# Kernel tuning notes

Hardware: AMD Instinct MI355X
Metric: run time of the kernel (lower is better)

Reference implementation:

```python
import jax, jax.numpy as jnp
import numpy as np
import math

S, D = 8192, 128

def setup_inputs() -> dict:
    key = jax.random.key(0)
    kq, kk, kv = jax.random.split(key, 3)
    return {
        "q": jax.random.normal(kq, (S, D), dtype=jnp.float32),
        "k": jax.random.normal(kk, (S, D), dtype=jnp.float32),
        "v": jax.random.normal(kv, (S, D), dtype=jnp.float32),
    }

def reference(q, k, v):
    # scores: [S, S]; scale by sqrt(d) as in the torch module
    scale = 1.0 / math.sqrt(q.shape[1])
    scores = (q @ k.T) * scale
    attn = jax.nn.softmax(scores, axis=-1)
    return attn @ v
```

## Files before the change

kernel.cpp:

```cpp
#include <hip/hip_runtime.h>
#include <hip/hip_bf16.h>

#define SEQ 8192
#define HD 128
#define BM 256
#define BN 64
#define NQT (SEQ / BM)
#define THREADS 1024

typedef __bf16 bf16_t;
typedef __bf16 bf16x2 __attribute__((ext_vector_type(2)));
typedef __bf16 bf16x8 __attribute__((ext_vector_type(8)));
typedef float f32x4 __attribute__((ext_vector_type(4)));
typedef float f32x16 __attribute__((ext_vector_type(16)));
typedef unsigned int u32x4 __attribute__((ext_vector_type(4)));

#if __has_builtin(__builtin_amdgcn_exp2f)
__device__ inline float exp2_fast(float x) { return __builtin_amdgcn_exp2f(x); }
#else
__device__ inline float exp2_fast(float x) { return exp2f(x); }
#endif

__device__ inline void load_lds16(const void* g, void* l) {
  __builtin_amdgcn_global_load_lds(
      (const __attribute__((address_space(1))) void*)g,
      (__attribute__((address_space(3))) void*)l, 16, 0, 0);
}

__global__ __launch_bounds__(256) void prep_kernel(const float* __restrict__ K,
                                                   const float* __restrict__ V,
                                                   bf16_t* __restrict__ Kb,
                                                   bf16_t* __restrict__ VT) {
  const int b = (int)blockIdx.x;
  const int tid = (int)threadIdx.x;
  if (b < 256) {
    __shared__ float tile[64][65];
    const int T = b & 127;
    const int d0 = (b >> 7) * 64;
    const int s0 = T * 64;
    const int r = tid >> 2;
    const int c0 = (tid & 3) * 16;
#pragma unroll
    for (int j4 = 0; j4 < 4; ++j4) {
      float4 x = *(const float4*)&V[(size_t)(s0 + r) * HD + d0 + c0 + j4 * 4];
      tile[r][c0 + j4 * 4 + 0] = x.x;
      tile[r][c0 + j4 * 4 + 1] = x.y;
      tile[r][c0 + j4 * 4 + 2] = x.z;
      tile[r][c0 + j4 * 4 + 3] = x.w;
    }
    __syncthreads();
    const int d_l = tid & 63;
    const int kc0 = (tid >> 6) * 2;
#pragma unroll
    for (int k2 = 0; k2 < 2; ++k2) {
      const int kc = kc0 + k2;
      bf16x8 wv;
#pragma unroll
      for (int j = 0; j < 8; ++j) wv[j] = (bf16_t)tile[kc * 8 + j][d_l];
      *(bf16x8*)&VT[((size_t)(T * 8 + kc) * 128 + d0 + d_l) * 8] = wv;
    }
  } else {
    const int base = (b - 256) * 2048 + tid * 8;
    const int row = base >> 7;
    const int c = (base >> 3) & 15;
    const int T = row >> 6;
    const int r = row & 63;
    float4 a = *(const float4*)&K[base];
    float4 cc = *(const float4*)&K[base + 4];
    bf16x8 f;
    f[0] = (bf16_t)a.x; f[1] = (bf16_t)a.y; f[2] = (bf16_t)a.z; f[3] = (bf16_t)a.w;
    f[4] = (bf16_t)cc.x; f[5] = (bf16_t)cc.y; f[6] = (bf16_t)cc.z; f[7] = (bf16_t)cc.w;
    *(bf16x8*)&Kb[((size_t)(T * 16 + c) * 64 + r) * 8] = f;
  }
}

__global__ __launch_bounds__(THREADS, 4) void fattn_kernel(
    const float* __restrict__ Q, const bf16_t* __restrict__ Kb,
    const bf16_t* __restrict__ VT, float* __restrict__ OpartT,
    float* __restrict__ Lpart, int kshift, int nit) {
  __shared__ __align__(16) bf16_t kt[2 * 8192];
  __shared__ __align__(16) bf16_t vt[3 * 8192];
  __shared__ __align__(16) char pbc[2 * 32768];

  const int tid = (int)threadIdx.x;
  const int lane = tid & 63;
  const int w = tid >> 6;
  const int qw = w & 7;
  const int g = w >> 3;
  const int h = lane >> 5;
  const int n32 = lane & 31;

  const int qt = (int)blockIdx.x >> kshift;
  const int sp = (int)blockIdx.x & ((1 << kshift) - 1);
  const int qbase = qt * BM;
  const int tile0 = sp * nit;

  const float SC2 = 0.08838834764831845f * 1.4426950408889634f;

  bf16x8 qf[8];
  {
    const float* qp = Q + (size_t)(qbase + qw * 32 + n32) * HD + h * 8;
#pragma unroll
    for (int kk = 0; kk < 8; ++kk) {
      float4 a = *(const float4*)(qp + kk * 16);
      float4 b = *(const float4*)(qp + kk * 16 + 4);
      bf16x8 f;
      f[0] = (bf16_t)(a.x * SC2); f[1] = (bf16_t)(a.y * SC2);
      f[2] = (bf16_t)(a.z * SC2); f[3] = (bf16_t)(a.w * SC2);
      f[4] = (bf16_t)(b.x * SC2); f[5] = (bf16_t)(b.y * SC2);
      f[6] = (bf16_t)(b.z * SC2); f[7] = (bf16_t)(b.w * SC2);
      qf[kk] = f;
    }
  }

  f32x16 o_acc[2];
#pragma unroll
  for (int i = 0; i < 2; ++i)
#pragma unroll
    for (int e = 0; e < 16; ++e) o_acc[i][e] = 0.f;
  float l_acc = 0.f;

  const bf16_t* ksrc = Kb + ((size_t)(tile0 * 16 + w) * 64 + lane) * 8;
  const bf16_t* vsrc = VT + ((size_t)(tile0 * 8 + (w >> 1)) * 128 + (w & 1) * 64 + lane) * 8;
  char* kdstb = (char*)kt + w * 1024;
  char* vdstb = (char*)vt + w * 1024;

  load_lds16(ksrc, kdstb);
  load_lds16(vsrc, vdstb);
  ksrc += 8192;
  vsrc += 8192;
  __syncthreads();

  const bf16_t* ktb = kt + (g * 32 + n32) * 8 + h * 512;
  const bf16_t* vtb = vt + (g * 64 + n32) * 8 + h * 1024;
  char* pbw = pbc + w * 2048 + lane * 16;
  const char* pbr = pbc + qw * 2048 + lane * 16;

  int kt_ro = 0;
  int ktd = 16384;
  int v_pv = 16384, v_nx = 0, v_fr = 8192;
  int p_wo = 0;

  for (int it = 0; it <= nit; ++it) {
    if (it + 1 < nit) {
      load_lds16(ksrc, kdstb + ktd);
      load_lds16(vsrc, vdstb + 2 * v_fr);
      ksrc += 8192;
      vsrc += 8192;
    }

    if (it < nit) {
      const bf16_t* kr = ktb + kt_ro;
      f32x16 sacc;
#pragma unroll
      for (int e = 0; e < 16; ++e) sacc[e] = 0.f;
#pragma unroll
      for (int kk = 0; kk < 8; ++kk) {
        bf16x8 af = *(const bf16x8*)(kr + kk * 1024);
        sacc = __builtin_amdgcn_mfma_f32_32x32x16_bf16(af, qf[kk], sacc, 0, 0, 0);
      }
#pragma unroll
      for (int kk2 = 0; kk2 < 2; ++kk2) {
        float pf[8];
#pragma unroll
        for (int j = 0; j < 8; ++j) pf[j] = exp2_fast(sacc[8 * kk2 + j]);
#pragma unroll
        for (int j = 0; j < 8; ++j) l_acc += pf[j];
        bf16x2 p0, p1, p2, p3;
        p0[0] = (bf16_t)pf[0]; p0[1] = (bf16_t)pf[1];
        p1[0] = (bf16_t)pf[2]; p1[1] = (bf16_t)pf[3];
        p2[0] = (bf16_t)pf[4]; p2[1] = (bf16_t)pf[5];
        p3[0] = (bf16_t)pf[6]; p3[1] = (bf16_t)pf[7];
        const unsigned int sA = __builtin_bit_cast(unsigned int, p0);
        const unsigned int sB = __builtin_bit_cast(unsigned int, p1);
        const unsigned int sC = __builtin_bit_cast(unsigned int, p2);
        const unsigned int sD = __builtin_bit_cast(unsigned int, p3);
        unsigned int s0 = h ? sA : sC, s1 = h ? sB : sD;
        unsigned int r0 = __shfl_xor(s0, 32);
        unsigned int r1 = __shfl_xor(s1, 32);
        unsigned int o0 = h ? sC : sA, o1 = h ? sD : sB;
        u32x4 fv;
        fv[0] = h ? r0 : o0; fv[1] = h ? r1 : o1;
        fv[2] = h ? o0 : r0; fv[3] = h ? o1 : r1;
        *(u32x4*)(pbw + p_wo + kk2 * 1024) = fv;
      }
    }

    if (it > 0) {
      const bf16_t* vr = vtb + v_pv;
      const char* pr = pbr + (p_wo ^ 32768);
#pragma unroll
      for (int c = 0; c < 4; ++c) {
        bf16x8 pb = *(const bf16x8*)(pr + (c >> 1) * 16384 + (c & 1) * 1024);
#pragma unroll
        for (int dt = 0; dt < 2; ++dt) {
          bf16x8 av = *(const bf16x8*)(vr + c * 2048 + dt * 256);
          o_acc[dt] = __builtin_amdgcn_mfma_f32_32x32x16_bf16(av, pb, o_acc[dt], 0, 0, 0);
        }
      }
    }

    if (it < nit) __syncthreads();

    kt_ro ^= 8192;
    ktd ^= 16384;
    int tswp = v_pv; v_pv = v_nx; v_nx = v_fr; v_fr = tswp;
    p_wo ^= 32768;
  }

  {
    float* op = OpartT + (size_t)sp * HD * SEQ + qbase + qw * 32 + n32;
#pragma unroll
    for (int dt = 0; dt < 2; ++dt)
#pragma unroll
      for (int reg = 0; reg < 16; ++reg) {
        const int d = g * 64 + dt * 32 + (reg & 3) + 8 * (reg >> 2) + 4 * h;
        op[(size_t)d * SEQ] = o_acc[dt][reg];
      }
    float l = l_acc + __shfl_xor(l_acc, 32);
    __syncthreads();
    float* lfb = (float*)pbc;
    if (lane < 32) lfb[g * 256 + qw * 32 + n32] = l;
    __syncthreads();
    if (g == 0 && lane < 32)
      Lpart[(size_t)sp * SEQ + qbase + qw * 32 + n32] =
          l + lfb[256 + qw * 32 + n32];
  }
}

__global__ __launch_bounds__(256) void combine_kernel(const float* __restrict__ OpartT,
                                                      const float* __restrict__ Lpart,
                                                      float* __restrict__ out, int ksplit) {
  __shared__ float tile[64][68];
  __shared__ float lbuf[64];
  const int tid = (int)threadIdx.x;
  const int q0 = (int)blockIdx.x * 64;
  if (tid < 64) {
    float s = 0.f;
    for (int sp = 0; sp < ksplit; ++sp) s += Lpart[(size_t)sp * SEQ + q0 + tid];
    lbuf[tid] = 1.0f / s;
  }
  __syncthreads();
  const int dd = tid >> 2, qc = tid & 3;
  const int q = tid >> 2, dc = tid & 3;
  for (int db = 0; db < 2; ++db) {
    f32x4 acc[4];
#pragma unroll
    for (int jj = 0; jj < 4; ++jj)
#pragma unroll
      for (int e = 0; e < 4; ++e) acc[jj][e] = 0.f;
    for (int sp = 0; sp < ksplit; ++sp) {
      const float* src = OpartT + ((size_t)sp * HD + db * 64 + dd) * SEQ + q0 + qc * 16;
#pragma unroll
      for (int jj = 0; jj < 4; ++jj) {
        f32x4 v = *(const f32x4*)(src + jj * 4);
#pragma unroll
        for (int e = 0; e < 4; ++e) acc[jj][e] += v[e];
      }
    }
#pragma unroll
    for (int jj = 0; jj < 4; ++jj) *(f32x4*)&tile[dd][qc * 16 + jj * 4] = acc[jj];
    __syncthreads();
    const float inv = lbuf[q];
#pragma unroll
    for (int jj = 0; jj < 4; ++jj) {
      f32x4 r;
#pragma unroll
      for (int i = 0; i < 4; ++i) r[i] = tile[dc * 16 + jj * 4 + i][q] * inv;
      *(f32x4*)&out[(size_t)(q0 + q) * HD + db * 64 + dc * 16 + jj * 4] = r;
    }
    __syncthreads();
  }
}

extern "C" void kernel_launch(void* const* d_in, const int* in_sizes, int n_in,
                              void* d_out, int out_size, void* d_ws, size_t ws_size,
                              hipStream_t stream) {
  const float* Q = (const float*)d_in[0];
  const float* K = (const float*)d_in[1];
  const float* V = (const float*)d_in[2];
  float* out = (float*)d_out;

  int ksplit = 8, kshift = 3;
  while (ksplit > 1) {
    size_t need = (size_t)ksplit * SEQ * HD * 4
                + (size_t)ksplit * SEQ * 4
                + (size_t)SEQ * HD * 2 * 2;
    if (need <= ws_size) break;
    ksplit >>= 1; kshift--;
  }

  char* ws = (char*)d_ws;
  float* OpartT = (float*)ws;
  float* Lpart = (float*)(ws + (size_t)ksplit * SEQ * HD * 4);
  bf16_t* Kb = (bf16_t*)(ws + (size_t)ksplit * SEQ * HD * 4 + (size_t)ksplit * SEQ * 4);
  bf16_t* VT = Kb + (size_t)SEQ * HD;

  const int nit = SEQ / (ksplit * BN);

  prep_kernel<<<768, 256, 0, stream>>>(K, V, Kb, VT);
  fattn_kernel<<<NQT * ksplit, THREADS, 0, stream>>>(Q, Kb, VT, OpartT, Lpart, kshift, nit);
  combine_kernel<<<SEQ / 64, 256, 0, stream>>>(OpartT, Lpart, out, ksplit);
}
```

Measured before the change: 122.4 us.

## Specialize warp groups into QK/softmax producers and PV consumers

The 16 waves were previously split into two groups that each computed half of QK^T plus softmax and half of the PV output dimensions. Now group 0 computes the full QK^T and exp for both key halves and writes P to LDS. Group 1 does all PV MFMAs across the full head dimension, one iteration behind. This removes the cross-group reduction of row sums at the end and balances MFMA work between the groups. In exchange, the producer holds only Q fragments and the consumer holds four output accumulators, which changes register pressure per role. Exp and pack work is no longer split, so it sits on one group's critical path.

```diff
diff --git a/kernel.cpp b/kernel.cpp
--- a/kernel.cpp
+++ b/kernel.cpp
@@ -86,7 +86,7 @@
   const int lane = tid & 63;
   const int w = tid >> 6;
   const int qw = w & 7;
-  const int g = w >> 3;
+  const int role = w >> 3;
   const int h = lane >> 5;
   const int n32 = lane & 31;
 
@@ -98,7 +98,7 @@
   const float SC2 = 0.08838834764831845f * 1.4426950408889634f;
 
   bf16x8 qf[8];
-  {
+  if (role == 0) {
     const float* qp = Q + (size_t)(qbase + qw * 32 + n32) * HD + h * 8;
 #pragma unroll
     for (int kk = 0; kk < 8; ++kk) {
@@ -113,9 +113,9 @@
     }
   }
 
-  f32x16 o_acc[2];
-#pragma unroll
-  for (int i = 0; i < 2; ++i)
+  f32x16 o_acc[4];
+#pragma unroll
+  for (int i = 0; i < 4; ++i)
 #pragma unroll
     for (int e = 0; e < 16; ++e) o_acc[i][e] = 0.f;
   float l_acc = 0.f;
@@ -131,9 +131,9 @@
   vsrc += 8192;
   __syncthreads();
 
-  const bf16_t* ktb = kt + (g * 32 + n32) * 8 + h * 512;
-  const bf16_t* vtb = vt + (g * 64 + n32) * 8 + h * 1024;
-  char* pbw = pbc + w * 2048 + lane * 16;
+  const bf16_t* ktb = kt + n32 * 8 + h * 512;
+  const bf16_t* vtb = vt + n32 * 8 + h * 1024;
+  char* pbw = pbc + qw * 2048 + lane * 16;
   const char* pbr = pbc + qw * 2048 + lane * 16;
 
   int kt_ro = 0;
@@ -149,53 +149,58 @@
       vsrc += 8192;
     }
 
-    if (it < nit) {
-      const bf16_t* kr = ktb + kt_ro;
-      f32x16 sacc;
-#pragma unroll
-      for (int e = 0; e < 16; ++e) sacc[e] = 0.f;
-#pragma unroll
-      for (int kk = 0; kk < 8; ++kk) {
-        bf16x8 af = *(const bf16x8*)(kr + kk * 1024);
-        sacc = __builtin_amdgcn_mfma_f32_32x32x16_bf16(af, qf[kk], sacc, 0, 0, 0);
+    if (role == 0) {
+      if (it < nit) {
+        const bf16_t* kr = ktb + kt_ro;
+#pragma unroll
+        for (int gg = 0; gg < 2; ++gg) {
+          f32x16 sacc;
+#pragma unroll
+          for (int e = 0; e < 16; ++e) sacc[e] = 0.f;
+#pragma unroll
+          for (int kk = 0; kk < 8; ++kk) {
+            bf16x8 af = *(const bf16x8*)(kr + gg * 256 + kk * 1024);
+            sacc = __builtin_amdgcn_mfma_f32_32x32x16_bf16(af, qf[kk], sacc, 0, 0, 0);
+          }
+#pragma unroll
+          for (int kk2 = 0; kk2 < 2; ++kk2) {
+            float pf[8];
+#pragma unroll
+            for (int j = 0; j < 8; ++j) pf[j] = exp2_fast(sacc[8 * kk2 + j]);
+#pragma unroll
+            for (int j = 0; j < 8; ++j) l_acc += pf[j];
+            bf16x2 p0, p1, p2, p3;
+            p0[0] = (bf16_t)pf[0]; p0[1] = (bf16_t)pf[1];
+            p1[0] = (bf16_t)pf[2]; p1[1] = (bf16_t)pf[3];
+            p2[0] = (bf16_t)pf[4]; p2[1] = (bf16_t)pf[5];
+            p3[0] = (bf16_t)pf[6]; p3[1] = (bf16_t)pf[7];
+            const unsigned int sA = __builtin_bit_cast(unsigned int, p0);
+            const unsigned int sB = __builtin_bit_cast(unsigned int, p1);
+            const unsigned int sC = __builtin_bit_cast(unsigned int, p2);
+            const unsigned int sD = __builtin_bit_cast(unsigned int, p3);
+            unsigned int s0 = h ? sA : sC, s1 = h ? sB : sD;
+            unsigned int r0 = __shfl_xor(s0, 32);
+            unsigned int r1 = __shfl_xor(s1, 32);
+            unsigned int o0 = h ? sC : sA, o1 = h ? sD : sB;
+            u32x4 fv;
+            fv[0] = h ? r0 : o0; fv[1] = h ? r1 : o1;
+            fv[2] = h ? o0 : r0; fv[3] = h ? o1 : r1;
+            *(u32x4*)(pbw + p_wo + gg * 16384 + kk2 * 1024) = fv;
+          }
+        }
       }
-#pragma unroll
-      for (int kk2 = 0; kk2 < 2; ++kk2) {
-        float pf[8];
-#pragma unroll
-        for (int j = 0; j < 8; ++j) pf[j] = exp2_fast(sacc[8 * kk2 + j]);
-#pragma unroll
-        for (int j = 0; j < 8; ++j) l_acc += pf[j];
-        bf16x2 p0, p1, p2, p3;
-        p0[0] = (bf16_t)pf[0]; p0[1] = (bf16_t)pf[1];
-        p1[0] = (bf16_t)pf[2]; p1[1] = (bf16_t)pf[3];
-        p2[0] = (bf16_t)pf[4]; p2[1] = (bf16_t)pf[5];
-        p3[0] = (bf16_t)pf[6]; p3[1] = (bf16_t)pf[7];
-        const unsigned int sA = __builtin_bit_cast(unsigned int, p0);
-        const unsigned int sB = __builtin_bit_cast(unsigned int, p1);
-        const unsigned int sC = __builtin_bit_cast(unsigned int, p2);
-        const unsigned int sD = __builtin_bit_cast(unsigned int, p3);
-        unsigned int s0 = h ? sA : sC, s1 = h ? sB : sD;
-        unsigned int r0 = __shfl_xor(s0, 32);
-        unsigned int r1 = __shfl_xor(s1, 32);
-        unsigned int o0 = h ? sC : sA, o1 = h ? sD : sB;
-        u32x4 fv;
-        fv[0] = h ? r0 : o0; fv[1] = h ? r1 : o1;
-        fv[2] = h ? o0 : r0; fv[3] = h ? o1 : r1;
-        *(u32x4*)(pbw + p_wo + kk2 * 1024) = fv;
-      }
-    }
-
-    if (it > 0) {
-      const bf16_t* vr = vtb + v_pv;
-      const char* pr = pbr + (p_wo ^ 32768);
-#pragma unroll
-      for (int c = 0; c < 4; ++c) {
-        bf16x8 pb = *(const bf16x8*)(pr + (c >> 1) * 16384 + (c & 1) * 1024);
-#pragma unroll
-        for (int dt = 0; dt < 2; ++dt) {
-          bf16x8 av = *(const bf16x8*)(vr + c * 2048 + dt * 256);
-          o_acc[dt] = __builtin_amdgcn_mfma_f32_32x32x16_bf16(av, pb, o_acc[dt], 0, 0, 0);
+    } else {
+      if (it > 0) {
+        const bf16_t* vr = vtb + v_pv;
+        const char* pr = pbr + (p_wo ^ 32768);
+#pragma unroll
+        for (int c = 0; c < 4; ++c) {
+          bf16x8 pb = *(const bf16x8*)(pr + (c >> 1) * 16384 + (c & 1) * 1024);
+#pragma unroll
+          for (int DT = 0; DT < 4; ++DT) {
+            bf16x8 av = *(const bf16x8*)(vr + c * 2048 + DT * 256);
+            o_acc[DT] = __builtin_amdgcn_mfma_f32_32x32x16_bf16(av, pb, o_acc[DT], 0, 0, 0);
+          }
         }
       }
     }
@@ -208,23 +213,19 @@
     p_wo ^= 32768;
   }
 
-  {
+  if (role == 1) {
     float* op = OpartT + (size_t)sp * HD * SEQ + qbase + qw * 32 + n32;
 #pragma unroll
-    for (int dt = 0; dt < 2; ++dt)
+    for (int DT = 0; DT < 4; ++DT)
 #pragma unroll
       for (int reg = 0; reg < 16; ++reg) {
-        const int d = g * 64 + dt * 32 + (reg & 3) + 8 * (reg >> 2) + 4 * h;
-        op[(size_t)d * SEQ] = o_acc[dt][reg];
+        const int d = DT * 32 + (reg & 3) + 8 * (reg >> 2) + 4 * h;
+        op[(size_t)d * SEQ] = o_acc[DT][reg];
       }
+  } else {
     float l = l_acc + __shfl_xor(l_acc, 32);
-    __syncthreads();
-    float* lfb = (float*)pbc;
-    if (lane < 32) lfb[g * 256 + qw * 32 + n32] = l;
-    __syncthreads();
-    if (g == 0 && lane < 32)
-      Lpart[(size_t)sp * SEQ + qbase + qw * 32 + n32] =
-          l + lfb[256 + qw * 32 + n32];
+    if (lane < 32)
+      Lpart[(size_t)sp * SEQ + qbase + qw * 32 + n32] = l;
   }
 }
 
```

New measurement: 157.7 us. +28.8%, slower.

## Permute K rows to drop P-fragment shuffles and stagger QK/PV order across waves

Applied to the files above, without the earlier changes.

The K preprocessing now writes rows in a permuted order within each 64-row tile. This makes the S accumulator layout from the QK MFMA line up with the B-operand layout PV needs, so the cross-half __shfl_xor exchange and selects when packing P to bf16 are removed. Separately, even waves run QK+exp then PV while odd waves run PV then QK+exp. The goal is to interleave MFMA-heavy and exp-heavy phases across the waves sharing a SIMD. The permutation must exactly match the MFMA output mapping, otherwise the results are wrong.

```diff
diff --git a/kernel.cpp b/kernel.cpp
--- a/kernel.cpp
+++ b/kernel.cpp
@@ -65,12 +65,13 @@
     const int c = (base >> 3) & 15;
     const int T = row >> 6;
     const int r = row & 63;
+    const int pr = (r & 0x33) | ((r & 4) << 1) | ((r & 8) >> 1);
     float4 a = *(const float4*)&K[base];
     float4 cc = *(const float4*)&K[base + 4];
     bf16x8 f;
     f[0] = (bf16_t)a.x; f[1] = (bf16_t)a.y; f[2] = (bf16_t)a.z; f[3] = (bf16_t)a.w;
     f[4] = (bf16_t)cc.x; f[5] = (bf16_t)cc.y; f[6] = (bf16_t)cc.z; f[7] = (bf16_t)cc.w;
-    *(bf16x8*)&Kb[((size_t)(T * 16 + c) * 64 + r) * 8] = f;
+    *(bf16x8*)&Kb[((size_t)(T * 16 + c) * 64 + pr) * 8] = f;
   }
 }
 
@@ -141,6 +142,48 @@
   int v_pv = 16384, v_nx = 0, v_fr = 8192;
   int p_wo = 0;
 
+  auto QKEXP = [&]() {
+    const bf16_t* kr = ktb + kt_ro;
+    f32x16 sacc;
+#pragma unroll
+    for (int e = 0; e < 16; ++e) sacc[e] = 0.f;
+#pragma unroll
+    for (int kk = 0; kk < 8; ++kk) {
+      bf16x8 af = *(const bf16x8*)(kr + kk * 1024);
+      sacc = __builtin_amdgcn_mfma_f32_32x32x16_bf16(af, qf[kk], sacc, 0, 0, 0);
+    }
+#pragma unroll
+    for (int kk2 = 0; kk2 < 2; ++kk2) {
+      float pf[8];
+#pragma unroll
+      for (int j = 0; j < 8; ++j) pf[j] = exp2_fast(sacc[8 * kk2 + j]);
+#pragma unroll
+      for (int j = 0; j < 8; ++j) l_acc += pf[j];
+      u32x4 fv;
+#pragma unroll
+      for (int p2 = 0; p2 < 4; ++p2) {
+        bf16x2 pp;
+        pp[0] = (bf16_t)pf[2 * p2 + 0];
+        pp[1] = (bf16_t)pf[2 * p2 + 1];
+        fv[p2] = __builtin_bit_cast(unsigned int, pp);
+      }
+      *(u32x4*)(pbw + p_wo + kk2 * 1024) = fv;
+    }
+  };
+  auto PV = [&]() {
+    const bf16_t* vr = vtb + v_pv;
+    const char* pr = pbr + (p_wo ^ 32768);
+#pragma unroll
+    for (int c = 0; c < 4; ++c) {
+      bf16x8 pb = *(const bf16x8*)(pr + (c >> 1) * 16384 + (c & 1) * 1024);
+#pragma unroll
+      for (int dt = 0; dt < 2; ++dt) {
+        bf16x8 av = *(const bf16x8*)(vr + c * 2048 + dt * 256);
+        o_acc[dt] = __builtin_amdgcn_mfma_f32_32x32x16_bf16(av, pb, o_acc[dt], 0, 0, 0);
+      }
+    }
+  };
+
   for (int it = 0; it <= nit; ++it) {
     if (it + 1 < nit) {
       load_lds16(ksrc, kdstb + ktd);
@@ -149,55 +192,12 @@
       vsrc += 8192;
     }
 
-    if (it < nit) {
-      const bf16_t* kr = ktb + kt_ro;
-      f32x16 sacc;
-#pragma unroll
-      for (int e = 0; e < 16; ++e) sacc[e] = 0.f;
-#pragma unroll
-      for (int kk = 0; kk < 8; ++kk) {
-        bf16x8 af = *(const bf16x8*)(kr + kk * 1024);
-        sacc = __builtin_amdgcn_mfma_f32_32x32x16_bf16(af, qf[kk], sacc, 0, 0, 0);
-      }
-#pragma unroll
-      for (int kk2 = 0; kk2 < 2; ++kk2) {
-        float pf[8];
-#pragma unroll
-        for (int j = 0; j < 8; ++j) pf[j] = exp2_fast(sacc[8 * kk2 + j]);
-#pragma unroll
-        for (int j = 0; j < 8; ++j) l_acc += pf[j];
-        bf16x2 p0, p1, p2, p3;
-        p0[0] = (bf16_t)pf[0]; p0[1] = (bf16_t)pf[1];
-        p1[0] = (bf16_t)pf[2]; p1[1] = (bf16_t)pf[3];
-        p2[0] = (bf16_t)pf[4]; p2[1] = (bf16_t)pf[5];
-        p3[0] = (bf16_t)pf[6]; p3[1] = (bf16_t)pf[7];
-        const unsigned int sA = __builtin_bit_cast(unsigned int, p0);
-        const unsigned int sB = __builtin_bit_cast(unsigned int, p1);
-        const unsigned int sC = __builtin_bit_cast(unsigned int, p2);
-        const unsigned int sD = __builtin_bit_cast(unsigned int, p3);
-        unsigned int s0 = h ? sA : sC, s1 = h ? sB : sD;
-        unsigned int r0 = __shfl_xor(s0, 32);
-        unsigned int r1 = __shfl_xor(s1, 32);
-        unsigned int o0 = h ? sC : sA, o1 = h ? sD : sB;
-        u32x4 fv;
-        fv[0] = h ? r0 : o0; fv[1] = h ? r1 : o1;
-        fv[2] = h ? o0 : r0; fv[3] = h ? o1 : r1;
-        *(u32x4*)(pbw + p_wo + kk2 * 1024) = fv;
-      }
-    }
-
-    if (it > 0) {
-      const bf16_t* vr = vtb + v_pv;
-      const char* pr = pbr + (p_wo ^ 32768);
-#pragma unroll
-      for (int c = 0; c < 4; ++c) {
-        bf16x8 pb = *(const bf16x8*)(pr + (c >> 1) * 16384 + (c & 1) * 1024);
-#pragma unroll
-        for (int dt = 0; dt < 2; ++dt) {
-          bf16x8 av = *(const bf16x8*)(vr + c * 2048 + dt * 256);
-          o_acc[dt] = __builtin_amdgcn_mfma_f32_32x32x16_bf16(av, pb, o_acc[dt], 0, 0, 0);
-        }
-      }
+    if ((w & 1) == 0) {
+      if (it < nit) QKEXP();
+      if (it > 0) PV();
+    } else {
+      if (it > 0) PV();
+      if (it < nit) QKEXP();
     }
 
     if (it < nit) __syncthreads();
```

Result: no change. 122.5 us (+0.0%).
